# Kernel tuning notes

Hardware: AMD Instinct MI355X
Metric: run time of the kernel (lower is better)

Reference implementation:

```python
import jax, jax.numpy as jnp
import numpy as np

V, E, ENC, DEC, OUT = 148, 256, 512, 1024, 80
B, T_TEXT, T_MEL = 32, 200, 400
H = ENC // 2  # per-direction encoder hidden


def lstm_cell(h, c, x, Wih, Whh, b):
    # PyTorch gate order: i, f, g, o; b = b_ih + b_hh
    gates = x @ Wih.T + h @ Whh.T + b
    i, f, g, o = jnp.split(gates, 4, axis=-1)
    c = jax.nn.sigmoid(f) * c + jax.nn.sigmoid(i) * jnp.tanh(g)
    h = jax.nn.sigmoid(o) * jnp.tanh(c)
    return h, c


def run_lstm(x_tbe, Wih, Whh, b, hsize):
    Bb = x_tbe.shape[1]
    def step(carry, x):
        h, c = lstm_cell(carry[0], carry[1], x, Wih, Whh, b)
        return (h, c), h
    init = (jnp.zeros((Bb, hsize), x_tbe.dtype), jnp.zeros((Bb, hsize), x_tbe.dtype))
    _, hs = jax.lax.scan(step, init, x_tbe)
    return hs  # (T, B, hsize)


def setup_inputs() -> dict:
    key = jax.random.key(0)
    ks = jax.random.split(key, 16)
    g = lambda k, s: jax.random.normal(k, s, jnp.float32) * 0.05
    return {
        "text_inputs": jax.random.randint(ks[0], (B, T_TEXT), 0, V),
        "mel_targets": jax.random.normal(ks[1], (B, T_MEL, OUT), jnp.float32),
        "emb": g(ks[2], (V, E)),
        "enc_f_Wih": g(ks[3], (4 * H, E)), "enc_f_Whh": g(ks[4], (4 * H, H)),
        "enc_f_b": jnp.zeros((4 * H,), jnp.float32),
        "enc_b_Wih": g(ks[5], (4 * H, E)), "enc_b_Whh": g(ks[6], (4 * H, H)),
        "enc_b_b": jnp.zeros((4 * H,), jnp.float32),
        "Ws": g(ks[7], (DEC, ENC + DEC)), "bs": jnp.zeros((DEC,), jnp.float32),
        "v": g(ks[8], (DEC,)),
        "dec_Wih": g(ks[9], (4 * DEC, OUT + ENC)), "dec_Whh": g(ks[10], (4 * DEC, DEC)),
        "dec_b": jnp.zeros((4 * DEC,), jnp.float32),
        "Wout": g(ks[11], (OUT, DEC)), "bout": jnp.zeros((OUT,), jnp.float32),
        "Wstop": g(ks[12], (1, DEC)), "bstop": jnp.zeros((1,), jnp.float32),
    }


def reference(text_inputs, mel_targets, emb, enc_f_Wih, enc_f_Whh, enc_f_b,
              enc_b_Wih, enc_b_Whh, enc_b_b, Ws, bs, v, dec_Wih, dec_Whh,
              dec_b, Wout, bout, Wstop, bstop):
    Bb = text_inputs.shape[0]
    x = emb[text_inputs]                              # (B, T_text, E)
    xt = x.transpose(1, 0, 2)                         # (T_text, B, E)
    hf = run_lstm(xt, enc_f_Wih, enc_f_Whh, enc_f_b, H)
    hb = run_lstm(xt[::-1], enc_b_Wih, enc_b_Whh, enc_b_b, H)[::-1]
    enc_out = jnp.concatenate([hf, hb], -1).transpose(1, 0, 2)  # (B, S, ENC)

    # split score_layer weight along concat axis; precompute encoder projection once
    Ws_enc, Ws_dec = Ws[:, :ENC], Ws[:, ENC:]
    proj_enc = jnp.einsum('bse,de->bsd', enc_out, Ws_enc) + bs  # (B, S, DEC)

    go = jnp.zeros((Bb, 1, OUT), mel_targets.dtype)
    dec_in = jnp.concatenate([go, mel_targets[:, :-1]], 1).transpose(1, 0, 2)  # (T_mel, B, OUT)

    def step(carry, x_t):
        h, c = carry
        energy = jnp.tanh(proj_enc + (h @ Ws_dec.T)[:, None, :])  # (B, S, DEC)
        scores = energy @ v                                        # (B, S)
        w = jax.nn.softmax(scores, axis=1)
        ctx = jnp.einsum('bs,bse->be', w, enc_out)                 # (B, ENC)
        h, c = lstm_cell(h, c, jnp.concatenate([x_t, ctx], 1), dec_Wih, dec_Whh, dec_b)
        mel = h @ Wout.T + bout
        stop = jax.nn.sigmoid(h @ Wstop.T + bstop)
        return (h, c), (mel, stop, w)

    init = (jnp.zeros((Bb, DEC), jnp.float32), jnp.zeros((Bb, DEC), jnp.float32))
    _, (mels, stops, aligns) = jax.lax.scan(step, init, dec_in)
    return (mels.transpose(1, 0, 2), stops.transpose(1, 0, 2), aligns.transpose(1, 0, 2))
```

## Files before the change

### kernel.cpp

```cpp
#include <hip/hip_runtime.h>

typedef unsigned short u16;
typedef short s8v __attribute__((ext_vector_type(8)));
typedef float f4v __attribute__((ext_vector_type(4)));

#define MFMA16 __builtin_amdgcn_mfma_f32_16x16x32_bf16
#define SCOPE_AGENT __HIP_MEMORY_SCOPE_AGENT

__device__ __forceinline__ float bf2f(u16 u) {
  union { unsigned int i; float f; } c; c.i = ((unsigned int)u) << 16; return c.f;
}
__device__ __forceinline__ u16 f2bf(float f) {
  union { float f; unsigned int i; } c; c.f = f;
  unsigned int i = c.i;
  unsigned int r = i + 0x7FFFu + ((i >> 16) & 1u);
  return (u16)(r >> 16);
}
__device__ __forceinline__ float sigm(float x) {
  float e = __builtin_amdgcn_exp2f(-1.44269504f * x);
  return __builtin_amdgcn_rcpf(1.0f + e);
}
__device__ __forceinline__ float tanh_(float x) {
  float e = __builtin_amdgcn_exp2f(2.88539009f * x);
  return 1.0f - 2.0f * __builtin_amdgcn_rcpf(e + 1.0f);
}
__device__ __forceinline__ void store_out(void* out, int mode, long idx, float v) {
  if (mode) ((float*)out)[idx] = v;
  else      ((u16*)out)[idx] = f2bf(v);
}

__device__ __forceinline__ unsigned long long ld64a(const void* p) {
  return __hip_atomic_load((const unsigned long long*)p, __ATOMIC_RELAXED, SCOPE_AGENT);
}
__device__ __forceinline__ s8v ld16a(const void* p) {
  union { unsigned long long u[2]; s8v v; } c;
  c.u[0] = ld64a(p);
  c.u[1] = ld64a((const char*)p + 8);
  return c.v;
}
__device__ __forceinline__ float ldfa(const float* p) {
  return __hip_atomic_load(p, __ATOMIC_RELAXED, SCOPE_AGENT);
}
__device__ __forceinline__ void stfa(float* p, float v) {
  __hip_atomic_store(p, v, __ATOMIC_RELAXED, SCOPE_AGENT);
}
__device__ __forceinline__ void stha(u16* p, u16 v) {
  __hip_atomic_store(p, v, __ATOMIC_RELAXED, SCOPE_AGENT);
}
__device__ __forceinline__ float dot4(unsigned long long u, const u16* w) {
  union { unsigned long long u; u16 h[4]; } c; c.u = u;
  return bf2f(c.h[0]) * bf2f(w[0]) + bf2f(c.h[1]) * bf2f(w[1]) +
         bf2f(c.h[2]) * bf2f(w[2]) + bf2f(c.h[3]) * bf2f(w[3]);
}

__global__ void k_detect(const u16* __restrict__ raw, int* __restrict__ flag) {
  __shared__ int cnt[256];
  int c = 0;
  for (int j = 0; j < 8; ++j) {
    int i = (threadIdx.x * 8 + j) * 2;
    int e = (raw[i] >> 7) & 0xFF;
    c += (e >= 130);
  }
  cnt[threadIdx.x] = c;
  __syncthreads();
  if (threadIdx.x == 0) {
    int s = 0;
    for (int i = 0; i < 256; ++i) s += cnt[i];
    *flag = (s > 64) ? 1 : 0;
  }
}

__global__ void k_conv(const void* __restrict__ src, u16* __restrict__ dst,
                       int n, const int* __restrict__ flag) {
  int mode = *flag;
  int i = blockIdx.x * blockDim.x + threadIdx.x;
  int st = gridDim.x * blockDim.x;
  if (mode) {
    const float* s = (const float*)src;
    for (; i < n; i += st) dst[i] = f2bf(s[i]);
  } else {
    const u16* s = (const u16*)src;
    for (; i < n; i += st) dst[i] = s[i];
  }
}

__global__ void k_zero(unsigned int* p, int n) {
  int i = blockIdx.x * blockDim.x + threadIdx.x;
  int st = gridDim.x * blockDim.x;
  for (; i < n; i += st) p[i] = 0u;
}

__device__ __forceinline__ void gsync(unsigned* bar, unsigned* sep, bool heavy) {
  __syncthreads();
  if (threadIdx.x == 0) {
    unsigned e = *sep;
    if (heavy) __threadfence();
    unsigned* leaf = bar + 128 + ((blockIdx.x & 15) << 6);
    if (__hip_atomic_fetch_add(leaf, 1u, __ATOMIC_RELAXED, SCOPE_AGENT) == e * 16u + 15u) {
      if (__hip_atomic_fetch_add(bar + 64, 1u, __ATOMIC_RELAXED, SCOPE_AGENT) == e * 16u + 15u)
        __hip_atomic_fetch_add(bar, 1u, __ATOMIC_RELAXED, SCOPE_AGENT);
    }
    while (__hip_atomic_load(bar, __ATOMIC_RELAXED, SCOPE_AGENT) <= e)
      __builtin_amdgcn_s_sleep(1);
    *sep = e + 1;
    if (heavy) __threadfence();
    asm volatile("" ::: "memory");
  }
  __syncthreads();
}

struct __align__(16) SMem {
  u16 W[26112];
  u16 proj[25600];
  u16 wsd[16384];
  u16 v[1024];
  float hp[1024];
  float exl[32];
  float gsc[2048];
  float cst[128];
  unsigned ep;
};

struct P {
  const int* text;
  const u16 *emb, *eWihF, *eWhhF, *ebF, *eWihB, *eWhhB, *ebB;
  const u16 *Ws, *bs, *vv, *dWih, *dWhh, *db, *Wout, *bout, *Wstop, *bstop, *mel;
  u16 *enc_out, *proj;
  float *hp, *ctx, *sumexp;
  u16 *h_f, *h_b, *h_dec;
  void* out;
  const int* flag;
  unsigned* bar;
};

__global__ void __launch_bounds__(256, 1) k_all(P p) {
  __shared__ SMem sm;
  const int tid = threadIdx.x;
  const int bk = blockIdx.x;
  const int lane = tid & 63;
  const int wv = tid >> 6;
  const int q = lane >> 4, l15 = lane & 15;
  const s8v zero8 = {0, 0, 0, 0, 0, 0, 0, 0};
  if (tid == 0) sm.ep = 0;
  const int mode = *p.flag;

  const int dirE = bk >> 7;
  const int mtE = (bk >> 6) & 1;
  const int j0E = (bk & 63) * 4;
  {
    const u16* Wih = dirE ? p.eWihB : p.eWihF;
    const u16* Whh = dirE ? p.eWhhB : p.eWhhF;
    for (int i = tid; i < 1024; i += 256) {
      int f = i >> 4, nl = i & 15;
      int row = (nl >> 2) * 256 + j0E + (nl & 3);
      int k = f * 8;
      const u16* src = (k < 256) ? (Wih + row * 256 + k) : (Whh + row * 256 + k - 256);
      *(s8v*)(sm.W + (size_t)i * 8) = *(const s8v*)src;
    }
    if (tid < 64) sm.cst[tid] = 0.f;
  }
  float ebias;
  {
    const u16* eb = dirE ? p.ebB : p.ebF;
    ebias = bf2f(eb[(l15 >> 2) * 256 + j0E + (l15 & 3)]);
  }
  __syncthreads();
  {
    u16* hbuf = dirE ? p.h_b : p.h_f;
    for (int stp = 0; stp < 200; ++stp) {
      int tb = dirE ? (199 - stp) : stp;
      const u16* hR = hbuf + (stp & 1) * 8192;
      u16* hW = hbuf + ((stp + 1) & 1) * 8192;
      {
        int m = mtE * 16 + l15;
        const u16* xrow = p.emb + (long)p.text[m * 200 + tb] * 256;
        const u16* hrow = hR + m * 256;
        f4v acc;
        float b0 = (wv == 0) ? ebias : 0.f;
        acc[0] = b0; acc[1] = b0; acc[2] = b0; acc[3] = b0;
        int k80 = wv * 128 + q * 8;
        s8v a0 = (k80 < 256)      ? *(const s8v*)(xrow + k80)      : ld16a(hrow + (k80 - 256));
        s8v a1 = (k80 + 32 < 256) ? *(const s8v*)(xrow + k80 + 32) : ld16a(hrow + (k80 + 32 - 256));
        s8v a2 = (k80 + 64 < 256) ? *(const s8v*)(xrow + k80 + 64) : ld16a(hrow + (k80 + 64 - 256));
        s8v a3 = (k80 + 96 < 256) ? *(const s8v*)(xrow + k80 + 96) : ld16a(hrow + (k80 + 96 - 256));
        const u16* wb = sm.W + (size_t)(((wv * 4) * 4 + q) * 16 + l15) * 8;
        acc = MFMA16(a0, *(const s8v*)(wb),        acc, 0, 0, 0);
        acc = MFMA16(a1, *(const s8v*)(wb + 512),  acc, 0, 0, 0);
        acc = MFMA16(a2, *(const s8v*)(wb + 1024), acc, 0, 0, 0);
        acc = MFMA16(a3, *(const s8v*)(wb + 1536), acc, 0, 0, 0);
#pragma unroll
        for (int r = 0; r < 4; ++r) sm.gsc[wv * 256 + (q * 4 + r) * 16 + l15] = acc[r];
      }
      __syncthreads();
      if (tid < 64) {
        int bl = tid >> 2, jj = tid & 3;
        float iG = 0.f, fG = 0.f, gG = 0.f, oG = 0.f;
#pragma unroll
        for (int w = 0; w < 4; ++w) {
          const float* g = sm.gsc + w * 256 + bl * 16;
          iG += g[jj]; fG += g[4 + jj]; gG += g[8 + jj]; oG += g[12 + jj];
        }
        float cold = sm.cst[tid];
        float cn = sigm(fG) * cold + sigm(iG) * tanh_(gG);
        float hn = sigm(oG) * tanh_(cn);
        sm.cst[tid] = cn;
        u16 hb16 = f2bf(hn);
        int b = mtE * 16 + bl;
        int col = j0E + jj;
        stha(&hW[b * 256 + col], hb16);
        p.enc_out[((long)b * 200 + tb) * 512 + dirE * 256 + col] = hb16;
      }
      gsync(p.bar, &sm.ep, stp == 199);
    }
  }

  {
    int w = bk * 4 + wv;
    for (int j = 0; j < 25; ++j) {
      int job = w * 25 + j;
      int mt = job >> 6, nt = job & 63;
      int m = mt * 16 + l15;
      const u16* arow = p.enc_out + (long)m * 512;
      int n = nt * 16 + l15;
      const u16* brow = p.Ws + (long)n * 1536;
      f4v acc = {0.f, 0.f, 0.f, 0.f};
#pragma unroll
      for (int kc = 0; kc < 16; ++kc) {
        s8v a = *(const s8v*)(arow + kc * 32 + q * 8);
        s8v b = *(const s8v*)(brow + kc * 32 + q * 8);
        acc = MFMA16(a, b, acc, 0, 0, 0);
      }
      float bias = bf2f(p.bs[n]);
#pragma unroll
      for (int r = 0; r < 4; ++r)
        p.proj[(long)(mt * 16 + q * 4 + r) * 1024 + n] = f2bf(acc[r] + bias);
    }
  }
  gsync(p.bar, &sm.ep, true);

  const int bA = bk >> 3, s0A = (bk & 7) * 25;
  float dbias;
  {
    int j0 = bk * 4;
    for (int i = tid; i < 3264; i += 256) {
      int f = i >> 4, nl = i & 15;
      long row = (long)(nl >> 2) * 1024 + j0 + (nl & 3);
      int k = f * 8;
      s8v val;
      if (k < 592)       val = *(const s8v*)(p.dWih + row * 592 + k);
      else if (k < 1616) val = *(const s8v*)(p.dWhh + row * 1024 + k - 592);
      else               val = zero8;
      *(s8v*)(sm.W + (size_t)i * 8) = val;
    }
    dbias = bf2f(p.db[(l15 >> 2) * 1024 + j0 + (l15 & 3)]);
    if (bk < 69) {
      const u16* base = (bk < 64) ? (p.Ws + 512) : p.Wout;
      long rstr = (bk < 64) ? 1536 : 1024;
      long r0 = (bk < 64) ? bk * 16 : (long)(bk - 64) * 16;
      for (int i = tid; i < 2048; i += 256) {
        int f = i >> 4, nl = i & 15;
        *(s8v*)(sm.wsd + (size_t)i * 8) = *(const s8v*)(base + (r0 + nl) * rstr + f * 8);
      }
    } else if (bk == 69) {
      if (tid < 128) *(s8v*)(sm.wsd + tid * 8) = *(const s8v*)(p.Wstop + tid * 8);
    }
    const u16* psrc = p.proj + (long)(bA * 200 + s0A) * 1024;
    for (int i = tid * 8; i < 25600; i += 2048)
      *(s8v*)(sm.proj + i) = *(const s8v*)(psrc + i);
    if (tid < 128) *(s8v*)(sm.v + tid * 8) = *(const s8v*)(p.vv + tid * 8);
    if (tid < 128) sm.cst[tid] = 0.f;
  }
  __syncthreads();

  for (int t = 0; t <= 400; ++t) {
    const u16* hR = p.h_dec + (t & 1) * 32768;
    u16* hW = p.h_dec + ((t + 1) & 1) * 32768;
    if (bk < 64) {
      if (t < 400) {
        int mtile = wv & 1, khalf = wv >> 1;
        int m = mtile * 16 + l15;
        const u16* arow = hR + m * 1024;
        f4v acc = {0.f, 0.f, 0.f, 0.f};
#pragma unroll
        for (int g = 0; g < 4; ++g) {
          const u16* ab = arow + (khalf * 16 + g * 4) * 32 + q * 8;
          s8v a0 = ld16a(ab);
          s8v a1 = ld16a(ab + 32);
          s8v a2 = ld16a(ab + 64);
          s8v a3 = ld16a(ab + 96);
          const u16* wb = sm.wsd + (size_t)(((khalf * 16 + g * 4) * 4 + q) * 16 + l15) * 8;
          acc = MFMA16(a0, *(const s8v*)(wb),        acc, 0, 0, 0);
          acc = MFMA16(a1, *(const s8v*)(wb + 512),  acc, 0, 0, 0);
          acc = MFMA16(a2, *(const s8v*)(wb + 1024), acc, 0, 0, 0);
          acc = MFMA16(a3, *(const s8v*)(wb + 1536), acc, 0, 0, 0);
        }
#pragma unroll
        for (int r = 0; r < 4; ++r) sm.gsc[wv * 512 + (q * 4 + r) * 16 + l15] = acc[r];
        __syncthreads();
        for (int oi = tid; oi < 512; oi += 256) {
          int mt2 = oi >> 8, idx = oi & 255;
          float val = sm.gsc[mt2 * 512 + idx] + sm.gsc[1024 + mt2 * 512 + idx];
          int mrow = mt2 * 16 + (idx >> 4);
          int n = bk * 16 + (idx & 15);
          stfa(&p.hp[mrow * 1024 + n], val);
        }
      }
    } else if (bk < 69) {
      if (t > 0) {
        int mtile = wv & 1, khalf = wv >> 1;
        int m = mtile * 16 + l15;
        const u16* arow = hR + m * 1024;
        f4v acc = {0.f, 0.f, 0.f, 0.f};
#pragma unroll
        for (int g = 0; g < 4; ++g) {
          const u16* ab = arow + (khalf * 16 + g * 4) * 32 + q * 8;
          s8v a0 = ld16a(ab);
          s8v a1 = ld16a(ab + 32);
          s8v a2 = ld16a(ab + 64);
          s8v a3 = ld16a(ab + 96);
          const u16* wb = sm.wsd + (size_t)(((khalf * 16 + g * 4) * 4 + q) * 16 + l15) * 8;
          acc = MFMA16(a0, *(const s8v*)(wb),        acc, 0, 0, 0);
          acc = MFMA16(a1, *(const s8v*)(wb + 512),  acc, 0, 0, 0);
          acc = MFMA16(a2, *(const s8v*)(wb + 1024), acc, 0, 0, 0);
          acc = MFMA16(a3, *(const s8v*)(wb + 1536), acc, 0, 0, 0);
        }
#pragma unroll
        for (int r = 0; r < 4; ++r) sm.gsc[wv * 512 + (q * 4 + r) * 16 + l15] = acc[r];
        __syncthreads();
        for (int oi = tid; oi < 512; oi += 256) {
          int mt2 = oi >> 8, idx = oi & 255;
          float val = sm.gsc[mt2 * 512 + idx] + sm.gsc[1024 + mt2 * 512 + idx];
          int mrow = mt2 * 16 + (idx >> 4);
          int n = (bk - 64) * 16 + (idx & 15);
          store_out(p.out, mode, ((long)mrow * 400 + (t - 1)) * 80 + n,
                    val + bf2f(p.bout[n]));
        }
      }
    } else if (bk == 69) {
      if (t > 0) {
        int b = tid >> 3, kp = tid & 7;
        const u16* hrow = hR + b * 1024 + kp * 128;
        float s = 0.f;
#pragma unroll
        for (int g = 0; g < 4; ++g) {
          const u16* hb = hrow + g * 32;
          const u16* wb = sm.wsd + kp * 128 + g * 32;
          unsigned long long u0 = ld64a(hb);
          unsigned long long u1 = ld64a(hb + 4);
          unsigned long long u2 = ld64a(hb + 8);
          unsigned long long u3 = ld64a(hb + 12);
          unsigned long long u4 = ld64a(hb + 16);
          unsigned long long u5 = ld64a(hb + 20);
          unsigned long long u6 = ld64a(hb + 24);
          unsigned long long u7 = ld64a(hb + 28);
          s += dot4(u0, wb)      + dot4(u1, wb + 4)  + dot4(u2, wb + 8)  + dot4(u3, wb + 12)
             + dot4(u4, wb + 16) + dot4(u5, wb + 20) + dot4(u6, wb + 24) + dot4(u7, wb + 28);
        }
        s += __shfl_xor(s, 1, 64);
        s += __shfl_xor(s, 2, 64);
        s += __shfl_xor(s, 4, 64);
        if (kp == 0)
          store_out(p.out, mode, 1024000 + (long)b * 400 + (t - 1),
                    sigm(s + bf2f(p.bstop[0])));
      }
    } else if (bk < 134) {
      stfa(&p.ctx[(bk - 70) * 256 + tid], 0.f);
    } else if (bk == 134) {
      if (tid < 32) stfa(&p.sumexp[tid], 0.f);
    }
    if (t == 400) break;
    gsync(p.bar, &sm.ep, false);

    {
      const float* hpb = p.hp + bA * 1024 + tid;
      float v0 = ldfa(hpb);
      float v1 = ldfa(hpb + 256);
      float v2 = ldfa(hpb + 512);
      float v3 = ldfa(hpb + 768);
      sm.hp[tid] = v0; sm.hp[tid + 256] = v1; sm.hp[tid + 512] = v2; sm.hp[tid + 768] = v3;
    }
    __syncthreads();
    {
      f4v h0a = *(const f4v*)(sm.hp + lane * 8);
      f4v h0b = *(const f4v*)(sm.hp + lane * 8 + 4);
      f4v h1a = *(const f4v*)(sm.hp + 512 + lane * 8);
      f4v h1b = *(const f4v*)(sm.hp + 512 + lane * 8 + 4);
      s8v v0 = *(const s8v*)(sm.v + lane * 8);
      s8v v1 = *(const s8v*)(sm.v + 512 + lane * 8);
      for (int si = wv; si < 25; si += 4) {
        const u16* prow = sm.proj + si * 1024;
        s8v p0 = *(const s8v*)(prow + lane * 8);
        s8v p1 = *(const s8v*)(prow + 512 + lane * 8);
        float part = 0.f;
#pragma unroll
        for (int jj = 0; jj < 4; ++jj) {
          part += tanh_(bf2f((u16)p0[jj]) + h0a[jj]) * bf2f((u16)v0[jj]);
          part += tanh_(bf2f((u16)p0[jj + 4]) + h0b[jj]) * bf2f((u16)v0[jj + 4]);
          part += tanh_(bf2f((u16)p1[jj]) + h1a[jj]) * bf2f((u16)v1[jj]);
          part += tanh_(bf2f((u16)p1[jj + 4]) + h1b[jj]) * bf2f((u16)v1[jj + 4]);
        }
#pragma unroll
        for (int off = 32; off >= 1; off >>= 1) part += __shfl_xor(part, off, 64);
        if (lane == 0) sm.exl[si] = __builtin_amdgcn_exp2f(1.44269504f * part);
      }
    }
    __syncthreads();
    if (tid == 0) {
      float ss = 0.f;
      for (int i = 0; i < 25; ++i) ss += sm.exl[i];
      atomicAdd(&p.sumexp[bA], ss);
    }
    {
      int e0 = tid * 2;
      const u16* eb = p.enc_out + (long)(bA * 200 + s0A) * 512 + e0;
      float a0 = 0.f, a1 = 0.f;
#pragma unroll 5
      for (int i = 0; i < 25; ++i) {
        float w = sm.exl[i];
        unsigned pr = *(const unsigned*)(eb + (size_t)i * 512);
        a0 += w * bf2f((u16)(pr & 0xffffu));
        a1 += w * bf2f((u16)(pr >> 16));
      }
      atomicAdd(&p.ctx[bA * 512 + e0], a0);
      atomicAdd(&p.ctx[bA * 512 + e0 + 1], a1);
    }
    gsync(p.bar, &sm.ep, false);

    {
      int mtile = wv & 1, khalf = wv >> 1;
      int m = mtile * 16 + l15;
      float rsm = __builtin_amdgcn_rcpf(ldfa(&p.sumexp[m]));
      const u16* melrow = p.mel + ((long)m * 400 + (t - 1)) * 80;
      const u16* hrow = hR + m * 1024;
      const float* crow = p.ctx + m * 512;
      auto gload = [&](int kc) -> s8v {
        int k8 = kc * 32 + q * 8;
        if (k8 < 80) {
          return (t == 0) ? zero8 : *(const s8v*)(melrow + k8);
        } else if (k8 < 592) {
          const float* cr = crow + (k8 - 80);
          union { unsigned long long u[4]; float f[8]; } cu;
          cu.u[0] = ld64a(cr);     cu.u[1] = ld64a(cr + 2);
          cu.u[2] = ld64a(cr + 4); cu.u[3] = ld64a(cr + 6);
          s8v t8;
#pragma unroll
          for (int jj = 0; jj < 8; ++jj) t8[jj] = (short)f2bf(cu.f[jj] * rsm);
          return t8;
        } else if (k8 < 1616) {
          return ld16a(hrow + (k8 - 592));
        }
        return zero8;
      };
      f4v acc;
      float b0 = (khalf == 0) ? dbias : 0.f;
      acc[0] = b0; acc[1] = b0; acc[2] = b0; acc[3] = b0;
      for (int kcg = khalf; kcg < 51; kcg += 8) {
        s8v a0 = gload(kcg);
        s8v a1 = (kcg + 2 < 51) ? gload(kcg + 2) : zero8;
        s8v a2 = (kcg + 4 < 51) ? gload(kcg + 4) : zero8;
        s8v a3 = (kcg + 6 < 51) ? gload(kcg + 6) : zero8;
        const u16* wb = sm.W + (size_t)((kcg * 4 + q) * 16 + l15) * 8;
        acc = MFMA16(a0, *(const s8v*)(wb), acc, 0, 0, 0);
        if (kcg + 2 < 51) acc = MFMA16(a1, *(const s8v*)(wb + 1024), acc, 0, 0, 0);
        if (kcg + 4 < 51) acc = MFMA16(a2, *(const s8v*)(wb + 2048), acc, 0, 0, 0);
        if (kcg + 6 < 51) acc = MFMA16(a3, *(const s8v*)(wb + 3072), acc, 0, 0, 0);
      }
#pragma unroll
      for (int r = 0; r < 4; ++r) sm.gsc[wv * 512 + (q * 4 + r) * 16 + l15] = acc[r];
    }
    __syncthreads();
    if (tid < 128) {
      int bl = tid >> 2, jj = tid & 3;
      int mt2 = bl >> 4;
      const float* g0 = sm.gsc + mt2 * 512 + (bl & 15) * 16;
      const float* g1 = g0 + 1024;
      float iG = g0[jj] + g1[jj];
      float fG = g0[4 + jj] + g1[4 + jj];
      float gG = g0[8 + jj] + g1[8 + jj];
      float oG = g0[12 + jj] + g1[12 + jj];
      float cold = sm.cst[tid];
      float cn = sigm(fG) * cold + sigm(iG) * tanh_(gG);
      float hn = sigm(oG) * tanh_(cn);
      sm.cst[tid] = cn;
      stha(&hW[(long)bl * 1024 + bk * 4 + jj], f2bf(hn));
    } else if (tid >= 192 && tid < 217) {
      int sl = tid - 192;
      float rs = __builtin_amdgcn_rcpf(ldfa(&p.sumexp[bA]));
      store_out(p.out, mode, 1036800 + ((long)bA * 400 + t) * 200 + s0A + sl,
                sm.exl[sl] * rs);
    }
    gsync(p.bar, &sm.ep, false);
  }
}

extern "C" void kernel_launch(void* const* d_in, const int* in_sizes, int n_in,
                              void* d_out, int out_size, void* d_ws, size_t ws_size,
                              hipStream_t stream) {
  char* p = (char*)d_ws;
  auto carve = [&](size_t bytes) -> char* {
    char* r = p;
    p += (bytes + 255) & ~(size_t)255;
    return r;
  };
  char* zbase = p;
  u16* h_f = (u16*)carve(2 * 8192 * 2);
  u16* h_b = (u16*)carve(2 * 8192 * 2);
  u16* h_dec = (u16*)carve(2 * 32768 * 2);
  unsigned* bar = (unsigned*)carve(8192);
  size_t zwords = (size_t)(p - zbase) / 4;
  int* flag = (int*)carve(256);
  static const int cvn[18] = {
      1024000, 37888, 262144, 262144, 1024, 262144, 262144, 1024,
      1572864, 1024, 1024, 2424832, 4194304, 4096, 81920, 80, 1024, 1 };
  u16* cv[18];
  for (int i = 0; i < 18; ++i) cv[i] = (u16*)carve((size_t)cvn[i] * 2);
  u16* enc_out = (u16*)carve(3276800ull * 2);
  u16* proj = (u16*)carve(6553600ull * 2);
  float* hp = (float*)carve(32768 * 4);
  float* ctx = (float*)carve(16384 * 4);
  float* sumexp = (float*)carve(64 * 4);

  hipLaunchKernelGGL(k_detect, dim3(1), dim3(256), 0, stream,
                     (const u16*)d_in[2], flag);
  for (int i = 0; i < 18; ++i) {
    int n = in_sizes[i + 1];
    int blocks = (n + 255) / 256; if (blocks > 128) blocks = 128;
    hipLaunchKernelGGL(k_conv, dim3(blocks), dim3(256), 0, stream,
                       (const void*)d_in[i + 1], cv[i], n, (const int*)flag);
  }
  hipLaunchKernelGGL(k_zero, dim3(96), dim3(256), 0, stream,
                     (unsigned int*)zbase, (int)zwords);

  P prm;
  prm.text = (const int*)d_in[0];
  prm.mel = cv[0];   prm.emb = cv[1];
  prm.eWihF = cv[2]; prm.eWhhF = cv[3]; prm.ebF = cv[4];
  prm.eWihB = cv[5]; prm.eWhhB = cv[6]; prm.ebB = cv[7];
  prm.Ws = cv[8];    prm.bs = cv[9];    prm.vv = cv[10];
  prm.dWih = cv[11]; prm.dWhh = cv[12]; prm.db = cv[13];
  prm.Wout = cv[14]; prm.bout = cv[15]; prm.Wstop = cv[16]; prm.bstop = cv[17];
  prm.enc_out = enc_out; prm.proj = proj;
  prm.hp = hp; prm.ctx = ctx; prm.sumexp = sumexp;
  prm.h_f = h_f; prm.h_b = h_b; prm.h_dec = h_dec;
  prm.out = d_out; prm.flag = flag; prm.bar = bar;
  void* kargs[] = { (void*)&prm };
  (void)hipLaunchCooperativeKernel((void*)k_all, dim3(256), dim3(256), kargs, 0, stream);
}
```

Before: 11.75 ms.

## Replace tree-counter grid barrier with per-block flag barrier and split MFMA accumulators

Swaps the hierarchical atomic-counter grid barrier for a flag-array barrier: each block publishes its epoch in its own slot and waits on the relevant slots in parallel, one thread per peer. The encoder steps now wait only on the 64 blocks of their own direction and M-tile group, instead of all 256. MFMA chains are also split across two accumulators to shorten dependent-MFMA latency. The cost is more polling loads per barrier, and the new barrier's memory ordering relies on relaxed atomics with fences only on heavy syncs.

Result: slower. 16.21 ms (+37.9%).

```diff
diff --git a/kernel.cpp b/kernel.cpp
--- a/kernel.cpp
+++ b/kernel.cpp
@@ -90,21 +90,22 @@
   for (; i < n; i += st) p[i] = 0u;
 }
 
-__device__ __forceinline__ void gsync(unsigned* bar, unsigned* sep, bool heavy) {
+__device__ __forceinline__ void gsyncF(unsigned* flags, unsigned* sep,
+                                       int base, int count, bool heavy) {
+  __syncthreads();
+  unsigned e = *sep;
+  if (threadIdx.x == 0) {
+    if (heavy) __threadfence();
+    __hip_atomic_store(&flags[blockIdx.x], e, __ATOMIC_RELAXED, SCOPE_AGENT);
+  }
+  if ((int)threadIdx.x < count) {
+    while (__hip_atomic_load(&flags[base + threadIdx.x], __ATOMIC_RELAXED, SCOPE_AGENT) < e)
+      __builtin_amdgcn_s_sleep(1);
+  }
   __syncthreads();
   if (threadIdx.x == 0) {
-    unsigned e = *sep;
-    if (heavy) __threadfence();
-    unsigned* leaf = bar + 128 + ((blockIdx.x & 15) << 6);
-    if (__hip_atomic_fetch_add(leaf, 1u, __ATOMIC_RELAXED, SCOPE_AGENT) == e * 16u + 15u) {
-      if (__hip_atomic_fetch_add(bar + 64, 1u, __ATOMIC_RELAXED, SCOPE_AGENT) == e * 16u + 15u)
-        __hip_atomic_fetch_add(bar, 1u, __ATOMIC_RELAXED, SCOPE_AGENT);
-    }
-    while (__hip_atomic_load(bar, __ATOMIC_RELAXED, SCOPE_AGENT) <= e)
-      __builtin_amdgcn_s_sleep(1);
     *sep = e + 1;
     if (heavy) __threadfence();
-    asm volatile("" ::: "memory");
   }
   __syncthreads();
 }
@@ -141,12 +142,13 @@
   const int wv = tid >> 6;
   const int q = lane >> 4, l15 = lane & 15;
   const s8v zero8 = {0, 0, 0, 0, 0, 0, 0, 0};
-  if (tid == 0) sm.ep = 0;
+  if (tid == 0) sm.ep = 1;
   const int mode = *p.flag;
 
   const int dirE = bk >> 7;
   const int mtE = (bk >> 6) & 1;
   const int j0E = (bk & 63) * 4;
+  const int grpE = bk & 192;
   {
     const u16* Wih = dirE ? p.eWihB : p.eWihF;
     const u16* Whh = dirE ? p.eWhhB : p.eWhhF;
@@ -210,7 +212,8 @@
         stha(&hW[b * 256 + col], hb16);
         p.enc_out[((long)b * 200 + tb) * 512 + dirE * 256 + col] = hb16;
       }
-      gsync(p.bar, &sm.ep, stp == 199);
+      if (stp < 199) gsyncF(p.bar, &sm.ep, grpE, 64, false);
+      else           gsyncF(p.bar, &sm.ep, 0, 256, true);
     }
   }
 
@@ -236,7 +239,7 @@
         p.proj[(long)(mt * 16 + q * 4 + r) * 1024 + n] = f2bf(acc[r] + bias);
     }
   }
-  gsync(p.bar, &sm.ep, true);
+  gsyncF(p.bar, &sm.ep, 0, 256, true);
 
   const int bA = bk >> 3, s0A = (bk & 7) * 25;
   float dbias;
@@ -280,7 +283,8 @@
         int mtile = wv & 1, khalf = wv >> 1;
         int m = mtile * 16 + l15;
         const u16* arow = hR + m * 1024;
-        f4v acc = {0.f, 0.f, 0.f, 0.f};
+        f4v accA = {0.f, 0.f, 0.f, 0.f};
+        f4v accB = {0.f, 0.f, 0.f, 0.f};
 #pragma unroll
         for (int g = 0; g < 4; ++g) {
           const u16* ab = arow + (khalf * 16 + g * 4) * 32 + q * 8;
@@ -289,13 +293,21 @@
           s8v a2 = ld16a(ab + 64);
           s8v a3 = ld16a(ab + 96);
           const u16* wb = sm.wsd + (size_t)(((khalf * 16 + g * 4) * 4 + q) * 16 + l15) * 8;
-          acc = MFMA16(a0, *(const s8v*)(wb),        acc, 0, 0, 0);
-          acc = MFMA16(a1, *(const s8v*)(wb + 512),  acc, 0, 0, 0);
-          acc = MFMA16(a2, *(const s8v*)(wb + 1024), acc, 0, 0, 0);
-          acc = MFMA16(a3, *(const s8v*)(wb + 1536), acc, 0, 0, 0);
-        }
-#pragma unroll
-        for (int r = 0; r < 4; ++r) sm.gsc[wv * 512 + (q * 4 + r) * 16 + l15] = acc[r];
+          if (g < 2) {
+            accA = MFMA16(a0, *(const s8v*)(wb),        accA, 0, 0, 0);
+            accA = MFMA16(a1, *(const s8v*)(wb + 512),  accA, 0, 0, 0);
+            accA = MFMA16(a2, *(const s8v*)(wb + 1024), accA, 0, 0, 0);
+            accA = MFMA16(a3, *(const s8v*)(wb + 1536), accA, 0, 0, 0);
+          } else {
+            accB = MFMA16(a0, *(const s8v*)(wb),        accB, 0, 0, 0);
+            accB = MFMA16(a1, *(const s8v*)(wb + 512),  accB, 0, 0, 0);
+            accB = MFMA16(a2, *(const s8v*)(wb + 1024), accB, 0, 0, 0);
+            accB = MFMA16(a3, *(const s8v*)(wb + 1536), accB, 0, 0, 0);
+          }
+        }
+#pragma unroll
+        for (int r = 0; r < 4; ++r)
+          sm.gsc[wv * 512 + (q * 4 + r) * 16 + l15] = accA[r] + accB[r];
         __syncthreads();
         for (int oi = tid; oi < 512; oi += 256) {
           int mt2 = oi >> 8, idx = oi & 255;
@@ -310,7 +322,8 @@
         int mtile = wv & 1, khalf = wv >> 1;
         int m = mtile * 16 + l15;
         const u16* arow = hR + m * 1024;
-        f4v acc = {0.f, 0.f, 0.f, 0.f};
+        f4v accA = {0.f, 0.f, 0.f, 0.f};
+        f4v accB = {0.f, 0.f, 0.f, 0.f};
 #pragma unroll
         for (int g = 0; g < 4; ++g) {
           const u16* ab = arow + (khalf * 16 + g * 4) * 32 + q * 8;
@@ -319,13 +332,21 @@
           s8v a2 = ld16a(ab + 64);
           s8v a3 = ld16a(ab + 96);
           const u16* wb = sm.wsd + (size_t)(((khalf * 16 + g * 4) * 4 + q) * 16 + l15) * 8;
-          acc = MFMA16(a0, *(const s8v*)(wb),        acc, 0, 0, 0);
-          acc = MFMA16(a1, *(const s8v*)(wb + 512),  acc, 0, 0, 0);
-          acc = MFMA16(a2, *(const s8v*)(wb + 1024), acc, 0, 0, 0);
-          acc = MFMA16(a3, *(const s8v*)(wb + 1536), acc, 0, 0, 0);
-        }
-#pragma unroll
-        for (int r = 0; r < 4; ++r) sm.gsc[wv * 512 + (q * 4 + r) * 16 + l15] = acc[r];
+          if (g < 2) {
+            accA = MFMA16(a0, *(const s8v*)(wb),        accA, 0, 0, 0);
+            accA = MFMA16(a1, *(const s8v*)(wb + 512),  accA, 0, 0, 0);
+            accA = MFMA16(a2, *(const s8v*)(wb + 1024), accA, 0, 0, 0);
+            accA = MFMA16(a3, *(const s8v*)(wb + 1536), accA, 0, 0, 0);
+          } else {
+            accB = MFMA16(a0, *(const s8v*)(wb),        accB, 0, 0, 0);
+            accB = MFMA16(a1, *(const s8v*)(wb + 512),  accB, 0, 0, 0);
+            accB = MFMA16(a2, *(const s8v*)(wb + 1024), accB, 0, 0, 0);
+            accB = MFMA16(a3, *(const s8v*)(wb + 1536), accB, 0, 0, 0);
+          }
+        }
+#pragma unroll
+        for (int r = 0; r < 4; ++r)
+          sm.gsc[wv * 512 + (q * 4 + r) * 16 + l15] = accA[r] + accB[r];
         __syncthreads();
         for (int oi = tid; oi < 512; oi += 256) {
           int mt2 = oi >> 8, idx = oi & 255;
@@ -369,7 +390,7 @@
       if (tid < 32) stfa(&p.sumexp[tid], 0.f);
     }
     if (t == 400) break;
-    gsync(p.bar, &sm.ep, false);
+    gsyncF(p.bar, &sm.ep, 0, 256, false);
 
     {
       const float* hpb = p.hp + bA * 1024 + tid;
@@ -424,7 +445,7 @@
       atomicAdd(&p.ctx[bA * 512 + e0], a0);
       atomicAdd(&p.ctx[bA * 512 + e0 + 1], a1);
     }
-    gsync(p.bar, &sm.ep, false);
+    gsyncF(p.bar, &sm.ep, 0, 256, false);
 
     {
       int mtile = wv & 1, khalf = wv >> 1;
@@ -451,22 +472,24 @@
         }
         return zero8;
       };
-      f4v acc;
+      f4v accA, accB;
       float b0 = (khalf == 0) ? dbias : 0.f;
-      acc[0] = b0; acc[1] = b0; acc[2] = b0; acc[3] = b0;
+      accA[0] = b0; accA[1] = b0; accA[2] = b0; accA[3] = b0;
+      accB[0] = 0.f; accB[1] = 0.f; accB[2] = 0.f; accB[3] = 0.f;
       for (int kcg = khalf; kcg < 51; kcg += 8) {
         s8v a0 = gload(kcg);
         s8v a1 = (kcg + 2 < 51) ? gload(kcg + 2) : zero8;
         s8v a2 = (kcg + 4 < 51) ? gload(kcg + 4) : zero8;
         s8v a3 = (kcg + 6 < 51) ? gload(kcg + 6) : zero8;
         const u16* wb = sm.W + (size_t)((kcg * 4 + q) * 16 + l15) * 8;
-        acc = MFMA16(a0, *(const s8v*)(wb), acc, 0, 0, 0);
-        if (kcg + 2 < 51) acc = MFMA16(a1, *(const s8v*)(wb + 1024), acc, 0, 0, 0);
-        if (kcg + 4 < 51) acc = MFMA16(a2, *(const s8v*)(wb + 2048), acc, 0, 0, 0);
-        if (kcg + 6 < 51) acc = MFMA16(a3, *(const s8v*)(wb + 3072), acc, 0, 0, 0);
-      }
-#pragma unroll
-      for (int r = 0; r < 4; ++r) sm.gsc[wv * 512 + (q * 4 + r) * 16 + l15] = acc[r];
+        accA = MFMA16(a0, *(const s8v*)(wb), accA, 0, 0, 0);
+        if (kcg + 2 < 51) accA = MFMA16(a1, *(const s8v*)(wb + 1024), accA, 0, 0, 0);
+        if (kcg + 4 < 51) accB = MFMA16(a2, *(const s8v*)(wb + 2048), accB, 0, 0, 0);
+        if (kcg + 6 < 51) accB = MFMA16(a3, *(const s8v*)(wb + 3072), accB, 0, 0, 0);
+      }
+#pragma unroll
+      for (int r = 0; r < 4; ++r)
+        sm.gsc[wv * 512 + (q * 4 + r) * 16 + l15] = accA[r] + accB[r];
     }
     __syncthreads();
     if (tid < 128) {
@@ -489,7 +512,7 @@
       store_out(p.out, mode, 1036800 + ((long)bA * 400 + t) * 200 + s0A + sl,
                 sm.exl[sl] * rs);
     }
-    gsync(p.bar, &sm.ep, false);
+    gsyncF(p.bar, &sm.ep, 0, 256, false);
   }
 }
 
```
